# Optimization experiments

Hardware: AMD Instinct MI355X
Metric: run time of the kernel (lower is better)

The kernel has to match this reference:

```python
import jax, jax.numpy as jnp
import numpy as np

L, N, HID, HEADS, BLK = 4096, 2, 1024, 16, 64
RAND_NUM = 2


def setup_inputs() -> dict:
    key = jax.random.key(0)
    ks = jax.random.split(key, 11)
    s = 0.02
    nb = L // BLK
    return {
        "query": jax.random.normal(ks[0], (L, N, HID), jnp.float32),
        "q_proj": jax.random.normal(ks[1], (HID, HID), jnp.float32) * s,
        "q_bias": jax.random.normal(ks[2], (HID,), jnp.float32) * s,
        "k_proj": jax.random.normal(ks[3], (HID, HID), jnp.float32) * s,
        "k_bias": jax.random.normal(ks[4], (HID,), jnp.float32) * s,
        "v_proj": jax.random.normal(ks[5], (HID, HID), jnp.float32) * s,
        "v_bias": jax.random.normal(ks[6], (HID,), jnp.float32) * s,
        "out_proj": jax.random.normal(ks[7], (HID, HID), jnp.float32) * s,
        "out_bias": jax.random.normal(ks[8], (HID,), jnp.float32) * s,
        "rand_indices": jax.random.randint(ks[9], (nb - 2, RAND_NUM), 2, nb, jnp.int64 if jax.config.jax_enable_x64 else jnp.int32),
        "h": HEADS,
        "block_size": BLK,
    }


def reference(query, q_proj, q_bias, k_proj, k_bias, v_proj, v_bias,
              out_proj, out_bias, rand_indices, h, block_size):
    Lq, Nb, hidden = query.shape
    dh = hidden // h
    b = block_size
    nb = Lq // b
    Z = Nb * h  # batch*heads leading dim
    scale = dh ** -0.5

    lin = lambda x, w, bi: x @ w.T + bi
    # [L, N, hidden] -> [N*h, L, dh]
    q = lin(query, q_proj, q_bias).reshape(Lq, Z, dh).transpose(1, 0, 2) * scale
    k = lin(query, k_proj, k_bias).reshape(Lq, Z, dh).transpose(1, 0, 2)
    v = lin(query, v_proj, v_bias).reshape(Lq, Z, dh).transpose(1, 0, 2)

    qb = q.reshape(Z, nb, b, dh)
    kb = k.reshape(Z, nb, b, dh)
    vb = v.reshape(Z, nb, b, dh)

    # ---- global blocks: first 2 blocks of queries attend to everything;
    #      all middle queries attend to first 2 key blocks ----
    head = jnp.einsum('zqd,zkd->zqk', q[:, :2 * b], k)          # [Z, 2b, L]
    col = jnp.einsum('zqd,zkd->zqk', q[:, 2 * b:], k[:, :2 * b])  # [Z, L-2b, 2b]

    # ---- sliding window (3 neighboring blocks), bottom row zero-padded ----
    skeys = jnp.concatenate([kb[:, 1:-2], kb[:, 2:-1], kb[:, 3:]], axis=2)  # [Z, nb-3, 3b, dh]
    sbot_k = jnp.concatenate([jnp.zeros_like(kb[:, -1:]), kb[:, -2:-1], kb[:, -1:]], axis=2)
    skeys = jnp.concatenate([skeys, sbot_k], axis=1)            # [Z, nb-2, 3b, dh]
    sqk = jnp.einsum('znqd,znkd->znqk', qb[:, 2:], skeys)
    sqk = sqk.reshape(Z, (nb - 2) * b, 3 * b)

    # ---- random blocks (rand_num per query block) ----
    gk = kb[:, rand_indices].reshape(Z, nb - 2, RAND_NUM * b, dh)
    rqk = jnp.einsum('znqd,znkd->znqk', qb[:, 2:], gk)
    rqk = rqk.reshape(Z, (nb - 2) * b, RAND_NUM * b)

    middle = jnp.concatenate([col, sqk, rqk], axis=-1)          # [Z, L-2b, 7b]

    head_attn = jax.nn.softmax(head, axis=-1)
    mid_attn = jax.nn.softmax(middle, axis=-1)

    # ---- attn @ v ----
    head_out = jnp.einsum('zqk,zkd->zqd', head_attn, v)          # [Z, 2b, dh]
    mid_out = jnp.einsum('zqk,zkd->zqd', mid_attn[:, :, :2 * b], v[:, :2 * b])

    svals = jnp.concatenate([vb[:, 1:-2], vb[:, 2:-1], vb[:, 3:]], axis=2)
    sbot_v = jnp.concatenate([vb[:, -2:-1], vb[:, -1:], jnp.zeros_like(vb[:, -1:])], axis=2)
    svals = jnp.concatenate([svals, sbot_v], axis=1)             # [Z, nb-2, 3b, dh]
    ms = mid_attn[:, :, 2 * b:5 * b].reshape(Z, nb - 2, b, 3 * b)
    mid_out = mid_out + jnp.einsum('znqk,znkd->znqd', ms, svals).reshape(Z, (nb - 2) * b, dh)

    gv = vb[:, rand_indices].reshape(Z, nb - 2, RAND_NUM * b, dh)
    mr = mid_attn[:, :, 5 * b:].reshape(Z, nb - 2, b, RAND_NUM * b)
    mid_out = mid_out + jnp.einsum('znqk,znkd->znqd', mr, gv).reshape(Z, (nb - 2) * b, dh)

    out = jnp.concatenate([head_out, mid_out], axis=1)           # [Z, L, dh]
    out = out.transpose(1, 0, 2).reshape(Lq, Nb, hidden)
    return lin(out, out_proj, out_bias)
```

## Files before the change

kernel.cpp:

```cpp
#include <hip/hip_runtime.h>
#include <stdint.h>

#define L_SEQ 4096
#define NBATCH 2
#define HID 1024
#define HEADS 16
#define DH 64
#define Z_DIM 32
#define NBLK 64
#define NROWS 8192
#define NSPLIT 8

typedef float f32x4 __attribute__((ext_vector_type(4)));
typedef short short8 __attribute__((ext_vector_type(8)));

typedef const uint32_t __attribute__((address_space(1))) *gas_ptr;
typedef uint32_t __attribute__((address_space(3))) *las_ptr;

__device__ __forceinline__ ushort f2bf(float f) {
  uint32_t u = __float_as_uint(f);
  uint32_t r = (u + 0x7FFFu + ((u >> 16) & 1u)) >> 16;
  return (ushort)r;
}

__device__ __forceinline__ void gload_lds16(const void* g, void* l) {
  __builtin_amdgcn_global_load_lds((gas_ptr)g, (las_ptr)l, 16, 0, 0);
}

__global__ void cvt_f32_bf16(const float* __restrict__ src, ushort* __restrict__ dst, int n4) {
  int i = blockIdx.x * blockDim.x + threadIdx.x;
  const int stride = gridDim.x * blockDim.x;
  for (; i < n4; i += stride) {
    float4 v = ((const float4*)src)[i];
    ushort4 o;
    o.x = f2bf(v.x); o.y = f2bf(v.y); o.z = f2bf(v.z); o.w = f2bf(v.w);
    ((ushort4*)dst)[i] = o;
  }
}

template <int FINAL>
__global__ __launch_bounds__(256)
void gemm_bt(const ushort* __restrict__ X,
             const ushort* __restrict__ W0, const ushort* __restrict__ W1,
             const ushort* __restrict__ W2,
             const float* __restrict__ b0, const float* __restrict__ b1,
             const float* __restrict__ b2,
             ushort* __restrict__ Qo, ushort* __restrict__ Ko,
             ushort* __restrict__ Vo, float* __restrict__ Fo) {
  const int tid = threadIdx.x;
  const int w = tid >> 6, l = tid & 63;
  const int lr = l & 15, lg = l >> 4;
  const int wr = w >> 1, wc = w & 1;

  const int total = FINAL ? 512 : 1536;
  const int per = total >> 3;
  const int f0 = blockIdx.x;
  const int nf = (f0 & 7) * per + (f0 >> 3);
  const int bx = nf & 7;
  const int by = (nf >> 3) & 63;
  const int zid = FINAL ? 0 : (nf >> 9);
  const int mbase = by * 128;
  const int nbase = bx * 128;

  const ushort* W = FINAL ? W0 : (zid == 0 ? W0 : (zid == 1 ? W1 : W2));
  const float*  B = FINAL ? b0 : (zid == 0 ? b0 : (zid == 1 ? b1 : b2));

  __shared__ ushort lds[8192];
  ushort* lA = lds;
  ushort* lB = lds + 4096;

  const int kch = (lg ^ (lr & 3)) << 3;

  f32x4 acc[4][4];
#pragma unroll
  for (int m = 0; m < 4; ++m)
#pragma unroll
    for (int n = 0; n < 4; ++n) acc[m][n] = (f32x4){0.f, 0.f, 0.f, 0.f};

  for (int k0 = 0; k0 < HID; k0 += 32) {
#pragma unroll
    for (int s = 0; s < 2; ++s) {
      const int chunk = s * 256 + tid;
      const int row = chunk >> 2, cc = chunk & 3;
      const int scc = cc ^ (row & 3);
      void* dstA = &lA[(s * 256 + (tid & ~63)) * 8];
      void* dstB = &lB[(s * 256 + (tid & ~63)) * 8];
      gload_lds16(X + (size_t)(mbase + row) * HID + k0 + scc * 8, dstA);
      gload_lds16(W + (size_t)(nbase + row) * HID + k0 + scc * 8, dstB);
    }
    __syncthreads();
    short8 af[4], bfr[4];
#pragma unroll
    for (int m = 0; m < 4; ++m)
      af[m] = *(const short8*)&lA[(wr * 64 + m * 16 + lr) * 32 + kch];
#pragma unroll
    for (int n = 0; n < 4; ++n)
      bfr[n] = *(const short8*)&lB[(wc * 64 + n * 16 + lr) * 32 + kch];
#pragma unroll
    for (int m = 0; m < 4; ++m)
#pragma unroll
      for (int n = 0; n < 4; ++n)
        acc[m][n] = __builtin_amdgcn_mfma_f32_16x16x32_bf16(af[m], bfr[n], acc[m][n], 0, 0, 0);
    __syncthreads();
  }

  if (FINAL) {
#pragma unroll
    for (int n = 0; n < 4; ++n) {
      const int col = nbase + wc * 64 + n * 16 + lr;
      const float bias = B[col];
#pragma unroll
      for (int m = 0; m < 4; ++m)
#pragma unroll
        for (int r = 0; r < 4; ++r) {
          const int row = mbase + wr * 64 + m * 16 + 4 * lg + r;
          Fo[(size_t)row * HID + col] = acc[m][n][r] + bias;
        }
    }
    return;
  }

  float biasn[4];
#pragma unroll
  for (int n = 0; n < 4; ++n) biasn[n] = B[nbase + wc * 64 + n * 16 + lr];

  if (zid == 2) {
#pragma unroll
    for (int nb2 = 0; nb2 < 2; ++nb2) {
#pragma unroll
      for (int ch = 0; ch < 2; ++ch) {
        __syncthreads();
        if (wc == ch) {
#pragma unroll
          for (int m = 0; m < 4; ++m)
#pragma unroll
            for (int n = 0; n < 4; ++n)
#pragma unroll
              for (int rr = 0; rr < 2; ++rr) {
                const int r = nb2 + 2 * rr;
                lds[(n * 16 + lr) * 72 + wr * 32 + m * 8 + 2 * lg + rr] =
                    f2bf(acc[m][n][r] + biasn[n]);
              }
        }
        __syncthreads();
        const int zz = nb2 * HEADS + (nbase >> 6) + ch;
#pragma unroll
        for (int it = 0; it < 2; ++it) {
          const int c = it * 256 + tid;
          const int colI = c >> 3, ls0 = (c & 7) * 8;
          const short8 v = *(const short8*)&lds[colI * 72 + ls0];
          *(short8*)&Vo[((size_t)zz * DH + colI) * L_SEQ + (mbase >> 1) + ls0] = v;
        }
      }
    }
  } else {
    ushort* Out = (zid == 0) ? Qo : Ko;
    const float sc = (zid == 0) ? 0.125f : 1.f;
#pragma unroll
    for (int nbp = 0; nbp < 2; ++nbp) {
#pragma unroll
      for (int hh = 0; hh < 2; ++hh) {
        __syncthreads();
        if (wc == hh) {
#pragma unroll
          for (int m = 0; m < 4; ++m)
#pragma unroll
            for (int n = 0; n < 4; ++n)
#pragma unroll
              for (int rr = 0; rr < 2; ++rr) {
                const int r = nbp + 2 * rr;
                lds[(wr * 32 + m * 8 + 2 * lg + rr) * 72 + n * 16 + lr] =
                    f2bf((acc[m][n][r] + biasn[n]) * sc);
              }
        }
        __syncthreads();
        const int zz = nbp * HEADS + (nbase >> 6) + hh;
#pragma unroll
        for (int it = 0; it < 2; ++it) {
          const int c = it * 256 + tid;
          const int lr2 = c >> 3, cc8 = c & 7;
          const short8 v = *(const short8*)&lds[lr2 * 72 + cc8 * 8];
          *(short8*)&Out[((size_t)zz * L_SEQ + (mbase >> 1) + lr2) * DH + cc8 * 8] = v;
        }
      }
    }
  }
}

__global__ __launch_bounds__(256)
void attn_sparse(const ushort* __restrict__ Q, const ushort* __restrict__ K,
                 const ushort* __restrict__ Vt, const int* __restrict__ rnd,
                 ushort* __restrict__ O,
                 float* __restrict__ Pp, float* __restrict__ Mp,
                 float* __restrict__ Lp) {
  const int bid = blockIdx.x;
  int z, qb, split = 0;
  bool head;
  if (bid < Z_DIM * 62) {
    z = bid / 62; qb = bid % 62 + 2; head = false;
  } else {
    const int t = bid - Z_DIM * 62;
    z = t >> 4; qb = (t >> 3) & 1; split = t & 7; head = true;
  }
  const int tid = threadIdx.x;
  const int w = tid >> 6, l = tid & 63;
  const int lr = l & 15, lg = l >> 4;

  __shared__ ushort Kl[64 * 64];
  __shared__ ushort Vl[64 * 64];
  __shared__ ushort Pl[4][16 * 64];

  const ushort* Qbase = Q + ((size_t)z * L_SEQ + qb * 64 + w * 16) * DH;
  const short8 aq0 = *(const short8*)(Qbase + lr * DH + lg * 8);
  const short8 aq1 = *(const short8*)(Qbase + lr * DH + 32 + lg * 8);

  float m[4], lsum[4];
  f32x4 accO[4];
#pragma unroll
  for (int r = 0; r < 4; ++r) { m[r] = -1e30f; lsum[r] = 0.f; }
#pragma unroll
  for (int t = 0; t < 4; ++t) accO[t] = (f32x4){0.f, 0.f, 0.f, 0.f};

  const int nslot = head ? 8 : 7;
  int sk[3] = {0, 0, 0}, sv[3] = {0, 0, 0}, rk0 = 0, rk1 = 0;
  if (!head) {
    const int i = qb - 2;
    rk0 = rnd[2 * i]; rk1 = rnd[2 * i + 1];
    if (qb < NBLK - 1) {
      sk[0] = qb - 1; sk[1] = qb; sk[2] = qb + 1;
      sv[0] = qb - 1; sv[1] = qb; sv[2] = qb + 1;
    } else {
      sk[0] = -1; sk[1] = NBLK - 2; sk[2] = NBLK - 1;
      sv[0] = NBLK - 2; sv[1] = NBLK - 1; sv[2] = -1;
    }
  }

  for (int slot = 0; slot < nslot; ++slot) {
    int ki, vi;
    if (head) { ki = split * 8 + slot; vi = ki; }
    else if (slot < 2) { ki = slot; vi = slot; }
    else if (slot < 5) { ki = sk[slot - 2]; vi = sv[slot - 2]; }
    else { ki = (slot == 5) ? rk0 : rk1; vi = ki; }

    if (slot) __syncthreads();
#pragma unroll
    for (int s = 0; s < 2; ++s) {
      const int chunk = s * 256 + tid;
      const int row = chunk >> 3, cc = chunk & 7;
      const int scc = cc ^ (row & 7);
      if (ki >= 0)
        gload_lds16(K + ((size_t)z * L_SEQ + ki * 64 + row) * DH + scc * 8,
                    &Kl[(s * 256 + (tid & ~63)) * 8]);
      if (vi >= 0)
        gload_lds16(Vt + ((size_t)z * DH + row) * L_SEQ + vi * 64 + scc * 8,
                    &Vl[(s * 256 + (tid & ~63)) * 8]);
    }
    __syncthreads();

    f32x4 sc[4];
    if (ki >= 0) {
#pragma unroll
      for (int t = 0; t < 4; ++t) {
        const int r = t * 16 + lr;
        const short8 b0 = *(const short8*)&Kl[r * 64 + ((lg ^ (r & 7)) << 3)];
        const short8 b1 = *(const short8*)&Kl[r * 64 + (((4 + lg) ^ (r & 7)) << 3)];
        f32x4 zz = (f32x4){0.f, 0.f, 0.f, 0.f};
        sc[t] = __builtin_amdgcn_mfma_f32_16x16x32_bf16(aq0, b0, zz, 0, 0, 0);
        sc[t] = __builtin_amdgcn_mfma_f32_16x16x32_bf16(aq1, b1, sc[t], 0, 0, 0);
      }
    } else {
#pragma unroll
      for (int t = 0; t < 4; ++t) sc[t] = (f32x4){0.f, 0.f, 0.f, 0.f};
    }

#pragma unroll
    for (int r = 0; r < 4; ++r) {
      float sm = fmaxf(fmaxf(sc[0][r], sc[1][r]), fmaxf(sc[2][r], sc[3][r]));
      sm = fmaxf(sm, __shfl_xor(sm, 1));
      sm = fmaxf(sm, __shfl_xor(sm, 2));
      sm = fmaxf(sm, __shfl_xor(sm, 4));
      sm = fmaxf(sm, __shfl_xor(sm, 8));
      const float mn = fmaxf(m[r], sm);
      const float scale = __expf(m[r] - mn);
      m[r] = mn;
      lsum[r] *= scale;
#pragma unroll
      for (int t = 0; t < 4; ++t) accO[t][r] *= scale;
      float psum = 0.f;
#pragma unroll
      for (int t = 0; t < 4; ++t) {
        const float p = __expf(sc[t][r] - mn);
        sc[t][r] = p;
        psum += p;
      }
      lsum[r] += psum;
    }

    if (vi >= 0) {
      ushort* P = &Pl[w][0];
#pragma unroll
      for (int t = 0; t < 4; ++t) {
#pragma unroll
        for (int r = 0; r < 4; ++r) {
          const int prow = 4 * lg + r, pcol = lr + 16 * t;
          P[prow * 64 + (((pcol >> 3) ^ (prow & 7)) << 3) + (pcol & 7)] = f2bf(sc[t][r]);
        }
      }
      const short8 ap0 = *(const short8*)&P[lr * 64 + ((lg ^ (lr & 7)) << 3)];
      const short8 ap1 = *(const short8*)&P[lr * 64 + (((4 + lg) ^ (lr & 7)) << 3)];
#pragma unroll
      for (int t = 0; t < 4; ++t) {
        const int r = t * 16 + lr;
        const short8 bv0 = *(const short8*)&Vl[r * 64 + ((lg ^ (r & 7)) << 3)];
        const short8 bv1 = *(const short8*)&Vl[r * 64 + (((4 + lg) ^ (r & 7)) << 3)];
        accO[t] = __builtin_amdgcn_mfma_f32_16x16x32_bf16(ap0, bv0, accO[t], 0, 0, 0);
        accO[t] = __builtin_amdgcn_mfma_f32_16x16x32_bf16(ap1, bv1, accO[t], 0, 0, 0);
      }
    }
  }

#pragma unroll
  for (int r = 0; r < 4; ++r) {
    float s = lsum[r];
    s += __shfl_xor(s, 1);
    s += __shfl_xor(s, 2);
    s += __shfl_xor(s, 4);
    s += __shfl_xor(s, 8);
    lsum[r] = s;
  }

  if (!head) {
    const int nb = z >> 4, hd = z & 15;
#pragma unroll
    for (int t = 0; t < 4; ++t) {
#pragma unroll
      for (int r = 0; r < 4; ++r) {
        const int lseq = qb * 64 + w * 16 + 4 * lg + r;
        O[((size_t)lseq * NBATCH + nb) * HID + hd * 64 + lr + 16 * t] =
            f2bf(accO[t][r] / lsum[r]);
      }
    }
  } else {
    const int hbase = (qb * Z_DIM + z) * NSPLIT + split;
#pragma unroll
    for (int t = 0; t < 4; ++t) {
#pragma unroll
      for (int r = 0; r < 4; ++r) {
        const int row = w * 16 + 4 * lg + r;
        Pp[((size_t)hbase * 64 + row) * 64 + lr + 16 * t] = accO[t][r];
      }
    }
    if (lr == 0) {
#pragma unroll
      for (int r = 0; r < 4; ++r) {
        const int row = w * 16 + 4 * lg + r;
        Mp[hbase * 64 + row] = m[r];
        Lp[hbase * 64 + row] = lsum[r];
      }
    }
  }
}

__global__ __launch_bounds__(256)
void head_reduce(const float* __restrict__ Pp, const float* __restrict__ Mp,
                 const float* __restrict__ Lp, ushort* __restrict__ O) {
  const int z = blockIdx.x >> 1, qb = blockIdx.x & 1;
  const int tid = threadIdx.x;
  const int row = tid >> 2, cg = tid & 3;
  const int base = (qb * Z_DIM + z) * NSPLIT;

  float mm[NSPLIT], wgt[NSPLIT];
  float mx = -1e30f;
#pragma unroll
  for (int s = 0; s < NSPLIT; ++s) {
    mm[s] = Mp[(base + s) * 64 + row];
    mx = fmaxf(mx, mm[s]);
  }
  float denom = 0.f;
#pragma unroll
  for (int s = 0; s < NSPLIT; ++s) {
    wgt[s] = __expf(mm[s] - mx);
    denom += Lp[(base + s) * 64 + row] * wgt[s];
  }
  const float inv = 1.f / denom;

  const int nb = z >> 4, hd = z & 15;
  const int lseq = qb * 64 + row;
#pragma unroll
  for (int c = 0; c < 16; ++c) {
    const int col = cg * 16 + c;
    float acc = 0.f;
#pragma unroll
    for (int s = 0; s < NSPLIT; ++s)
      acc += Pp[((size_t)(base + s) * 64 + row) * 64 + col] * wgt[s];
    O[((size_t)lseq * NBATCH + nb) * HID + hd * 64 + col] = f2bf(acc * inv);
  }
}

extern "C" void kernel_launch(void* const* d_in, const int* in_sizes, int n_in,
                              void* d_out, int out_size, void* d_ws, size_t ws_size,
                              hipStream_t stream) {
  (void)in_sizes; (void)n_in; (void)out_size; (void)ws_size;
  const float* query    = (const float*)d_in[0];
  const float* q_proj   = (const float*)d_in[1];
  const float* q_bias   = (const float*)d_in[2];
  const float* k_proj   = (const float*)d_in[3];
  const float* k_bias   = (const float*)d_in[4];
  const float* v_proj   = (const float*)d_in[5];
  const float* v_bias   = (const float*)d_in[6];
  const float* out_proj = (const float*)d_in[7];
  const float* out_bias = (const float*)d_in[8];
  const int*   rnd      = (const int*)d_in[9];

  ushort* Xb  = (ushort*)d_ws;
  ushort* Wq  = Xb + (size_t)NROWS * HID;
  ushort* Wk  = Wq + (size_t)HID * HID;
  ushort* Wv  = Wk + (size_t)HID * HID;
  ushort* Wo  = Wv + (size_t)HID * HID;
  ushort* Qb  = Wo + (size_t)HID * HID;
  ushort* Kb  = Qb + (size_t)Z_DIM * L_SEQ * DH;
  ushort* Vtb = Kb + (size_t)Z_DIM * L_SEQ * DH;
  float*  Pp  = (float*)(Vtb + (size_t)Z_DIM * DH * L_SEQ);
  float*  Mp  = Pp + (size_t)2 * Z_DIM * NSPLIT * 64 * 64;
  float*  Lp  = Mp + (size_t)2 * Z_DIM * NSPLIT * 64;
  ushort* Ob  = Xb;
  float*  Fo  = (float*)d_out;

  cvt_f32_bf16<<<2048, 256, 0, stream>>>(query, Xb, NROWS * HID / 4);
  cvt_f32_bf16<<<1024, 256, 0, stream>>>(q_proj, Wq, HID * HID / 4);
  cvt_f32_bf16<<<1024, 256, 0, stream>>>(k_proj, Wk, HID * HID / 4);
  cvt_f32_bf16<<<1024, 256, 0, stream>>>(v_proj, Wv, HID * HID / 4);
  cvt_f32_bf16<<<1024, 256, 0, stream>>>(out_proj, Wo, HID * HID / 4);

  gemm_bt<0><<<1536, 256, 0, stream>>>(
      Xb, Wq, Wk, Wv, q_bias, k_bias, v_bias, Qb, Kb, Vtb, nullptr);

  attn_sparse<<<Z_DIM * 62 + 2 * Z_DIM * NSPLIT, 256, 0, stream>>>(
      Qb, Kb, Vtb, rnd, Ob, Pp, Mp, Lp);

  head_reduce<<<2 * Z_DIM, 256, 0, stream>>>(Pp, Mp, Lp, Ob);

  gemm_bt<1><<<512, 256, 0, stream>>>(
      Ob, Wo, nullptr, nullptr, out_bias, nullptr, nullptr,
      nullptr, nullptr, nullptr, Fo);
}
```

Baseline: 188.1 us.

## Double-buffer GEMM LDS loads, change swizzle, and merge conversion kernels

The projection GEMM now double-buffers its LDS tiles, issuing global_load_lds for tile t+2 while computing tile t, with explicit vmcnt waits and barriers in place of the two syncthreads per iteration. The LDS XOR swizzle now keys on row>>1 rather than row to change the bank-conflict pattern. The five f32-to-bf16 conversion launches are merged into one kernel with one element per thread. LDS use per block doubles, which may reduce occupancy, and the hand-written waitcnt counts must match the number of loads issued per stage.

```diff
diff --git a/kernel.cpp b/kernel.cpp
--- a/kernel.cpp
+++ b/kernel.cpp
@@ -27,15 +27,28 @@
   __builtin_amdgcn_global_load_lds((gas_ptr)g, (las_ptr)l, 16, 0, 0);
 }
 
-__global__ void cvt_f32_bf16(const float* __restrict__ src, ushort* __restrict__ dst, int n4) {
-  int i = blockIdx.x * blockDim.x + threadIdx.x;
-  const int stride = gridDim.x * blockDim.x;
-  for (; i < n4; i += stride) {
-    float4 v = ((const float4*)src)[i];
-    ushort4 o;
-    o.x = f2bf(v.x); o.y = f2bf(v.y); o.z = f2bf(v.z); o.w = f2bf(v.w);
-    ((ushort4*)dst)[i] = o;
-  }
+__global__ __launch_bounds__(256)
+void cvt_multi(const float* __restrict__ s0, ushort* __restrict__ d0,
+               const float* __restrict__ s1, ushort* __restrict__ d1,
+               const float* __restrict__ s2, ushort* __restrict__ d2,
+               const float* __restrict__ s3, ushort* __restrict__ d3,
+               const float* __restrict__ s4, ushort* __restrict__ d4) {
+  const int i = blockIdx.x * blockDim.x + threadIdx.x;
+  const int NQ = NROWS * HID / 4;
+  const float4* src; ushort4* dst; int off;
+  if (i < NQ) {
+    src = (const float4*)s0; dst = (ushort4*)d0; off = i;
+  } else {
+    const int j = i - NQ;
+    const int r = j >> 18;
+    off = j & ((1 << 18) - 1);
+    src = (const float4*)(r == 0 ? s1 : r == 1 ? s2 : r == 2 ? s3 : s4);
+    dst = (ushort4*)(r == 0 ? d1 : r == 1 ? d2 : r == 2 ? d3 : d4);
+  }
+  float4 v = src[off];
+  ushort4 o;
+  o.x = f2bf(v.x); o.y = f2bf(v.y); o.z = f2bf(v.z); o.w = f2bf(v.w);
+  dst[off] = o;
 }
 
 template <int FINAL>
@@ -65,11 +78,9 @@
   const ushort* W = FINAL ? W0 : (zid == 0 ? W0 : (zid == 1 ? W1 : W2));
   const float*  B = FINAL ? b0 : (zid == 0 ? b0 : (zid == 1 ? b1 : b2));
 
-  __shared__ ushort lds[8192];
-  ushort* lA = lds;
-  ushort* lB = lds + 4096;
-
-  const int kch = (lg ^ (lr & 3)) << 3;
+  __shared__ ushort lds[2][8192];
+
+  const int kch = (lg ^ ((lr >> 1) & 3)) << 3;
 
   f32x4 acc[4][4];
 #pragma unroll
@@ -77,18 +88,20 @@
 #pragma unroll
     for (int n = 0; n < 4; ++n) acc[m][n] = (f32x4){0.f, 0.f, 0.f, 0.f};
 
-  for (int k0 = 0; k0 < HID; k0 += 32) {
+  auto stage = [&](int k0, int buf) {
 #pragma unroll
     for (int s = 0; s < 2; ++s) {
       const int chunk = s * 256 + tid;
       const int row = chunk >> 2, cc = chunk & 3;
-      const int scc = cc ^ (row & 3);
-      void* dstA = &lA[(s * 256 + (tid & ~63)) * 8];
-      void* dstB = &lB[(s * 256 + (tid & ~63)) * 8];
-      gload_lds16(X + (size_t)(mbase + row) * HID + k0 + scc * 8, dstA);
-      gload_lds16(W + (size_t)(nbase + row) * HID + k0 + scc * 8, dstB);
-    }
-    __syncthreads();
+      const int scc = cc ^ ((row >> 1) & 3);
+      gload_lds16(X + (size_t)(mbase + row) * HID + k0 + scc * 8,
+                  &lds[buf][(s * 256 + (tid & ~63)) * 8]);
+      gload_lds16(W + (size_t)(nbase + row) * HID + k0 + scc * 8,
+                  &lds[buf][4096 + (s * 256 + (tid & ~63)) * 8]);
+    }
+  };
+
+  auto compute_tile = [&](const ushort* lA, const ushort* lB) {
     short8 af[4], bfr[4];
 #pragma unroll
     for (int m = 0; m < 4; ++m)
@@ -101,7 +114,20 @@
 #pragma unroll
       for (int n = 0; n < 4; ++n)
         acc[m][n] = __builtin_amdgcn_mfma_f32_16x16x32_bf16(af[m], bfr[n], acc[m][n], 0, 0, 0);
-    __syncthreads();
+  };
+
+  stage(0, 0);
+  stage(32, 1);
+  for (int t = 0; t < 32; ++t) {
+    if (t < 30) { asm volatile("s_waitcnt vmcnt(4)" ::: "memory"); }
+    else        { asm volatile("s_waitcnt vmcnt(0)" ::: "memory"); }
+    __builtin_amdgcn_s_barrier();
+    __builtin_amdgcn_sched_barrier(0);
+    compute_tile(&lds[t & 1][0], &lds[t & 1][4096]);
+    __builtin_amdgcn_sched_barrier(0);
+    asm volatile("s_waitcnt lgkmcnt(0)" ::: "memory");
+    __builtin_amdgcn_s_barrier();
+    if (t < 30) stage((t + 2) * 32, t & 1);
   }
 
   if (FINAL) {
@@ -123,6 +149,7 @@
   float biasn[4];
 #pragma unroll
   for (int n = 0; n < 4; ++n) biasn[n] = B[nbase + wc * 64 + n * 16 + lr];
+  ushort* st = &lds[0][0];
 
   if (zid == 2) {
 #pragma unroll
@@ -138,7 +165,7 @@
 #pragma unroll
               for (int rr = 0; rr < 2; ++rr) {
                 const int r = nb2 + 2 * rr;
-                lds[(n * 16 + lr) * 72 + wr * 32 + m * 8 + 2 * lg + rr] =
+                st[(n * 16 + lr) * 72 + wr * 32 + m * 8 + 2 * lg + rr] =
                     f2bf(acc[m][n][r] + biasn[n]);
               }
         }
@@ -148,7 +175,7 @@
         for (int it = 0; it < 2; ++it) {
           const int c = it * 256 + tid;
           const int colI = c >> 3, ls0 = (c & 7) * 8;
-          const short8 v = *(const short8*)&lds[colI * 72 + ls0];
+          const short8 v = *(const short8*)&st[colI * 72 + ls0];
           *(short8*)&Vo[((size_t)zz * DH + colI) * L_SEQ + (mbase >> 1) + ls0] = v;
         }
       }
@@ -169,7 +196,7 @@
 #pragma unroll
               for (int rr = 0; rr < 2; ++rr) {
                 const int r = nbp + 2 * rr;
-                lds[(wr * 32 + m * 8 + 2 * lg + rr) * 72 + n * 16 + lr] =
+                st[(wr * 32 + m * 8 + 2 * lg + rr) * 72 + n * 16 + lr] =
                     f2bf((acc[m][n][r] + biasn[n]) * sc);
               }
         }
@@ -179,7 +206,7 @@
         for (int it = 0; it < 2; ++it) {
           const int c = it * 256 + tid;
           const int lr2 = c >> 3, cc8 = c & 7;
-          const short8 v = *(const short8*)&lds[lr2 * 72 + cc8 * 8];
+          const short8 v = *(const short8*)&st[lr2 * 72 + cc8 * 8];
           *(short8*)&Out[((size_t)zz * L_SEQ + (mbase >> 1) + lr2) * DH + cc8 * 8] = v;
         }
       }
@@ -426,11 +453,8 @@
   ushort* Ob  = Xb;
   float*  Fo  = (float*)d_out;
 
-  cvt_f32_bf16<<<2048, 256, 0, stream>>>(query, Xb, NROWS * HID / 4);
-  cvt_f32_bf16<<<1024, 256, 0, stream>>>(q_proj, Wq, HID * HID / 4);
-  cvt_f32_bf16<<<1024, 256, 0, stream>>>(k_proj, Wk, HID * HID / 4);
-  cvt_f32_bf16<<<1024, 256, 0, stream>>>(v_proj, Wv, HID * HID / 4);
-  cvt_f32_bf16<<<1024, 256, 0, stream>>>(out_proj, Wo, HID * HID / 4);
+  cvt_multi<<<(NROWS * HID / 4 + 4 * HID * HID / 4) / 256, 256, 0, stream>>>(
+      query, Xb, q_proj, Wq, k_proj, Wk, v_proj, Wv, out_proj, Wo);
 
   gemm_bt<0><<<1536, 256, 0, stream>>>(
       Xb, Wq, Wk, Wv, q_bias, k_bias, v_bias, Qb, Kb, Vtb, nullptr);
```

Result: faster. 172.4 us (-8.3%).
